# Kernel tuning notes

Hardware: AMD Instinct MI355X
Metric: run time of the kernel (lower is better)

The kernel has to match this reference:

```python
import jax, jax.numpy as jnp
import numpy as np

B, T, E = 2048, 200, 128
H1, H2 = 64, 32
NEG_INF = -(2.0 ** 32) + 1.0  # matches tf source's -2**32 + 1 padding value


def setup_inputs() -> dict:
    key = jax.random.key(0)
    ks = jax.random.split(key, 8)
    queries = jax.random.normal(ks[0], (B, E), dtype=jnp.float32)
    keys = jax.random.normal(ks[1], (B, T, E), dtype=jnp.float32)
    keys_id = jax.random.randint(ks[2], (B, T), 0, 2, dtype=jnp.int32)
    # Dense params: MLP input is concat([q,k,q-k,q*k]) -> 4*E = 512
    W1 = jax.random.normal(ks[3], (4 * E, H1), dtype=jnp.float32) * (1.0 / np.sqrt(4 * E))
    b1 = jnp.zeros((H1,), dtype=jnp.float32)
    W2 = jax.random.normal(ks[4], (H1, H2), dtype=jnp.float32) * (1.0 / np.sqrt(H1))
    b2 = jnp.zeros((H2,), dtype=jnp.float32)
    W3 = jax.random.normal(ks[5], (H2, 1), dtype=jnp.float32) * (1.0 / np.sqrt(H2))
    b3 = jnp.zeros((1,), dtype=jnp.float32)
    return {"queries": queries, "keys": keys, "keys_id": keys_id,
            "W1": W1, "b1": b1, "W2": W2, "b2": b2, "W3": W3, "b3": b3}


def reference(queries, keys, keys_id, W1, b1, W2, b2, W3, b3):
    # tile query over the time axis: [B,E] -> [B,T,E]
    q = jnp.broadcast_to(queries[:, None, :], keys.shape)
    # concat features: [B,T,4E]
    feat = jnp.concatenate([q, keys, q - keys, q * keys], axis=2)
    # small MLP scorer
    h = jax.nn.relu(jnp.einsum('btf,fh->bth', feat, W1) + b1)
    h = jax.nn.relu(jnp.einsum('bth,hk->btk', h, W2) + b2)
    weight = jnp.einsum('btk,ko->bto', h, W3) + b3  # [B,T,1]
    # masked softmax over time axis (padding id == 0)
    mask = (keys_id != 0)[:, :, None]  # [B,T,1]
    weight = jnp.where(mask, weight, jnp.float32(NEG_INF))
    weight = jax.nn.softmax(weight, axis=1)
    # weighted mean pooling (original uses reduce_mean, i.e. sum/T)
    return jnp.mean(weight * keys, axis=1)  # [B,E]
```

## Files before the change

### kernel.cpp

```cpp
#include <hip/hip_runtime.h>
#include <hip/hip_bf16.h>

#define NEG_INF_F (-4294967295.0f)

typedef __attribute__((ext_vector_type(8))) short bf16x8;
typedef __attribute__((ext_vector_type(4))) float f32x4;

__device__ __forceinline__ unsigned short f2bf(float x) {
    unsigned u = __float_as_uint(x);
    return (unsigned short)((u + 0x7fffu + ((u >> 16) & 1u)) >> 16);
}
__device__ __forceinline__ unsigned f2bf2(float a, float b) {
    __hip_bfloat162 h2 = __float22bfloat162_rn(make_float2(a, b));
    unsigned r; __builtin_memcpy(&r, &h2, 4); return r;
}
union FragU { unsigned u[4]; bf16x8 h; };

struct __align__(16) Smem {
    unsigned short Mt[64 * 128];
    unsigned short h1s[4][16 * 64];
    float q[128];
    float cpart[256];
    float Om[4][128];
    float mw[4], lw[4];
};

__global__ __launch_bounds__(256, 3)
void attn_fused(const float* __restrict__ Q,
                const float* __restrict__ Kg,
                const int*   __restrict__ kid,
                const float* __restrict__ W1,
                const float* __restrict__ b1,
                const float* __restrict__ W2,
                const float* __restrict__ b2,
                const float* __restrict__ W3,
                const float* __restrict__ b3,
                float* __restrict__ out)
{
    __shared__ Smem sm;
    const int b    = blockIdx.x;
    const int tid  = threadIdx.x;
    const int wave = tid >> 6;
    const int lane = tid & 63;
    const int l15  = lane & 15;
    const int quad = lane >> 4;

    if (tid < 128) sm.q[tid] = Q[b * 128 + tid];

    bf16x8 W2f[2][2];
    #pragma unroll
    for (int ks = 0; ks < 2; ++ks) {
        #pragma unroll
        for (int nt = 0; nt < 2; ++nt) {
            const int n = nt * 16 + l15;
            const int kb = ks * 32 + quad * 8;
            bf16x8 f;
            #pragma unroll
            for (int j = 0; j < 8; ++j) f[j] = (short)f2bf(W2[(kb + j) * 32 + n]);
            W2f[ks][nt] = f;
        }
    }
    const float w3a = W3[l15],  w3b = W3[16 + l15];
    const float b2a = b2[l15],  b2b = b2[16 + l15];
    const float b3v = b3[0];
    __syncthreads();

    {
        const int n  = tid & 63;
        const int ko = (tid >> 6) * 2;
        #pragma unroll
        for (int i = 0; i < 16; ++i) {
            const int k = i * 8 + ko;
            const float v0 = (W1[(128 + k) * 64 + n] - W1[(256 + k) * 64 + n])
                           + sm.q[k] * W1[(384 + k) * 64 + n];
            const float v1 = (W1[(129 + k) * 64 + n] - W1[(257 + k) * 64 + n])
                           + sm.q[k + 1] * W1[(385 + k) * 64 + n];
            const int g = (k >> 3) ^ (n & 15);
            *reinterpret_cast<unsigned*>(&sm.Mt[n * 128 + g * 8 + (k & 7)]) = f2bf2(v0, v1);
        }
    }
    {
        const int n = tid & 63, kc = tid >> 6;
        float acc = (kc == 0) ? b1[n] : 0.0f;
        #pragma unroll 4
        for (int i = 0; i < 32; ++i) {
            const int k = kc * 32 + i;
            acc += sm.q[k] * (W1[k * 64 + n] + W1[(256 + k) * 64 + n]);
        }
        sm.cpart[kc * 64 + n] = acc;
    }
    __syncthreads();

    float cn[4];
    #pragma unroll
    for (int nt = 0; nt < 4; ++nt) {
        const int n = nt * 16 + l15;
        cn[nt] = sm.cpart[n] + sm.cpart[64 + n] + sm.cpart[128 + n] + sm.cpart[192 + n];
    }

    const float* kbase = Kg + (size_t)b * 25600;
    unsigned short* h1w = &sm.h1s[wave][0];
    const f32x4 zero4 = {0.f, 0.f, 0.f, 0.f};

    float O[32];
    #pragma unroll
    for (int i = 0; i < 32; ++i) O[i] = 0.0f;
    float mrun = -__builtin_inff(), lrun = 0.0f;

    for (int tile = wave; tile < 13; tile += 4) {
        const int t0 = tile * 16;
        const int t  = t0 + l15;
        const int tr = min(t, 199);
        const float* kr = kbase + tr * 128;
        float4 ka[4], kb_[4];
        #pragma unroll
        for (int ks = 0; ks < 4; ++ks) {
            ka[ks]  = *reinterpret_cast<const float4*>(kr + ks * 32 + quad * 8);
            kb_[ks] = *reinterpret_cast<const float4*>(kr + ks * 32 + quad * 8 + 4);
        }
        const int kidv = kid[b * 200 + tr];

        f32x4 acc[4] = {zero4, zero4, zero4, zero4};
        #pragma unroll
        for (int ks = 0; ks < 4; ++ks) {
            FragU A;
            A.u[0] = f2bf2(ka[ks].x,  ka[ks].y);
            A.u[1] = f2bf2(ka[ks].z,  ka[ks].w);
            A.u[2] = f2bf2(kb_[ks].x, kb_[ks].y);
            A.u[3] = f2bf2(kb_[ks].z, kb_[ks].w);
            #pragma unroll
            for (int nt = 0; nt < 4; ++nt) {
                const int n = nt * 16 + l15;
                const int g = (ks * 4 + quad) ^ l15;
                const bf16x8 Bf = *reinterpret_cast<const bf16x8*>(&sm.Mt[n * 128 + g * 8]);
                acc[nt] = __builtin_amdgcn_mfma_f32_16x16x32_bf16(A.h, Bf, acc[nt], 0, 0, 0);
            }
        }
        #pragma unroll
        for (int nt = 0; nt < 4; ++nt) {
            const int n = nt * 16 + l15;
            #pragma unroll
            for (int r = 0; r < 4; ++r) {
                const int m = quad * 4 + r;
                const float h = fmaxf(acc[nt][r] + cn[nt], 0.0f);
                const int g = (n >> 3) ^ (m & 7);
                h1w[m * 64 + g * 8 + (n & 7)] = f2bf(h);
            }
        }
        f32x4 p0 = zero4, p1 = zero4;
        #pragma unroll
        for (int ks = 0; ks < 2; ++ks) {
            const int g = (ks * 4 + quad) ^ (l15 & 7);
            const bf16x8 A2l = *reinterpret_cast<const bf16x8*>(&h1w[l15 * 64 + g * 8]);
            p0 = __builtin_amdgcn_mfma_f32_16x16x32_bf16(A2l, W2f[ks][0], p0, 0, 0, 0);
            p1 = __builtin_amdgcn_mfma_f32_16x16x32_bf16(A2l, W2f[ks][1], p1, 0, 0, 0);
        }
        float sv[4];
        #pragma unroll
        for (int r = 0; r < 4; ++r)
            sv[r] = fmaxf(p0[r] + b2a, 0.f) * w3a + fmaxf(p1[r] + b2b, 0.f) * w3b;
        #pragma unroll
        for (int off = 1; off < 16; off <<= 1) {
            #pragma unroll
            for (int r = 0; r < 4; ++r) sv[r] += __shfl_xor(sv[r], off);
        }
        const int src = (l15 >> 2) * 16;
        const float s0 = __shfl(sv[0], src), s1 = __shfl(sv[1], src);
        const float s2 = __shfl(sv[2], src), s3 = __shfl(sv[3], src);
        const int rr = l15 & 3;
        const float sres = (rr == 0) ? s0 : (rr == 1) ? s1 : (rr == 2) ? s2 : s3;
        float x;
        if (t < 200) x = (kidv != 0) ? (sres + b3v) : NEG_INF_F;
        else         x = -__builtin_inff();
        float tmax = x;
        #pragma unroll
        for (int off = 1; off < 16; off <<= 1) tmax = fmaxf(tmax, __shfl_xor(tmax, off));
        const float mnew  = fmaxf(mrun, tmax);
        const float alpha = __expf(mrun - mnew);
        const float w     = __expf(x - mnew);
        float tsum = w;
        #pragma unroll
        for (int off = 1; off < 16; off <<= 1) tsum += __shfl_xor(tsum, off);
        lrun = lrun * alpha + tsum;
        mrun = mnew;
        #pragma unroll
        for (int ks = 0; ks < 4; ++ks) {
            O[ks*8+0] = fmaf(O[ks*8+0], alpha, w * ka[ks].x);
            O[ks*8+1] = fmaf(O[ks*8+1], alpha, w * ka[ks].y);
            O[ks*8+2] = fmaf(O[ks*8+2], alpha, w * ka[ks].z);
            O[ks*8+3] = fmaf(O[ks*8+3], alpha, w * ka[ks].w);
            O[ks*8+4] = fmaf(O[ks*8+4], alpha, w * kb_[ks].x);
            O[ks*8+5] = fmaf(O[ks*8+5], alpha, w * kb_[ks].y);
            O[ks*8+6] = fmaf(O[ks*8+6], alpha, w * kb_[ks].z);
            O[ks*8+7] = fmaf(O[ks*8+7], alpha, w * kb_[ks].w);
        }
    }

    #pragma unroll
    for (int off = 1; off < 16; off <<= 1) {
        #pragma unroll
        for (int i = 0; i < 32; ++i) O[i] += __shfl_xor(O[i], off);
    }
    if (l15 == 0) {
        #pragma unroll
        for (int ks = 0; ks < 4; ++ks) {
            *reinterpret_cast<float4*>(&sm.Om[wave][ks * 32 + quad * 8]) =
                make_float4(O[ks*8+0], O[ks*8+1], O[ks*8+2], O[ks*8+3]);
            *reinterpret_cast<float4*>(&sm.Om[wave][ks * 32 + quad * 8 + 4]) =
                make_float4(O[ks*8+4], O[ks*8+5], O[ks*8+6], O[ks*8+7]);
        }
    }
    if (lane == 0) { sm.mw[wave] = mrun; sm.lw[wave] = lrun; }
    __syncthreads();

    if (tid < 128) {
        const float M = fmaxf(fmaxf(sm.mw[0], sm.mw[1]), fmaxf(sm.mw[2], sm.mw[3]));
        float den = 0.f, val = 0.f;
        #pragma unroll
        for (int w = 0; w < 4; ++w) {
            const float a = __expf(sm.mw[w] - M);
            den += sm.lw[w] * a;
            val += sm.Om[w][tid] * a;
        }
        out[(size_t)b * 128 + tid] = val / (den * 200.0f);
    }
}

extern "C" void kernel_launch(void* const* d_in, const int* in_sizes, int n_in,
                              void* d_out, int out_size, void* d_ws, size_t ws_size,
                              hipStream_t stream) {
    (void)in_sizes; (void)n_in; (void)out_size; (void)d_ws; (void)ws_size;
    attn_fused<<<dim3(2048), dim3(256), 0, stream>>>(
        (const float*)d_in[0], (const float*)d_in[1], (const int*)d_in[2],
        (const float*)d_in[3], (const float*)d_in[4], (const float*)d_in[5],
        (const float*)d_in[6], (const float*)d_in[7], (const float*)d_in[8],
        (float*)d_out);
}
```

Measured before the change: 325.7 us.

## Split per-batch W1 folding into a precompute kernel and prefetch next key tile

The per-batch folded weight matrix (bf16, swizzled) and bias vector are now computed in a separate kernel and written to workspace. The main kernel copies them into LDS with vectorized loads instead of recomputing them from W1. The main loop also double-buffers the key tile in registers, loading the next tile before computing on the current one to hide global memory latency. The cost is a 16 KB per-batch round trip through global memory, a second kernel launch, and higher register pressure under a 3-waves occupancy bound.

```diff
diff --git a/kernel.cpp b/kernel.cpp
--- a/kernel.cpp
+++ b/kernel.cpp
@@ -16,26 +16,72 @@
 }
 union FragU { unsigned u[4]; bf16x8 h; };
 
+struct SmemA { float q[128]; float cpart[256]; };
+
+__global__ __launch_bounds__(256)
+void precompute_cm(const float* __restrict__ Q, const float* __restrict__ W1,
+                   const float* __restrict__ b1,
+                   float* __restrict__ c_all, unsigned short* __restrict__ M_all)
+{
+    __shared__ SmemA sm;
+    const int b = blockIdx.x;
+    const int tid = threadIdx.x;
+    if (tid < 128) sm.q[tid] = Q[b * 128 + tid];
+    __syncthreads();
+
+    {
+        const int n = tid & 63, kc = tid >> 6;
+        float acc = (kc == 0) ? b1[n] : 0.0f;
+        #pragma unroll 4
+        for (int i = 0; i < 32; ++i) {
+            const int k = kc * 32 + i;
+            acc += sm.q[k] * (W1[k * 64 + n] + W1[(256 + k) * 64 + n]);
+        }
+        sm.cpart[kc * 64 + n] = acc;
+    }
+
+    #pragma unroll
+    for (int i = 0; i < 4; ++i) {
+        const int pos = tid + i * 256;
+        const int n   = pos >> 4;
+        const int p   = pos & 15;
+        const int kb  = (p ^ (n & 15)) * 8;
+        unsigned u[4];
+        #pragma unroll
+        for (int j = 0; j < 4; ++j) {
+            const int k0 = kb + 2 * j, k1 = k0 + 1;
+            const float v0 = (W1[(128 + k0) * 64 + n] - W1[(256 + k0) * 64 + n])
+                           + sm.q[k0] * W1[(384 + k0) * 64 + n];
+            const float v1 = (W1[(128 + k1) * 64 + n] - W1[(256 + k1) * 64 + n])
+                           + sm.q[k1] * W1[(384 + k1) * 64 + n];
+            u[j] = f2bf2(v0, v1);
+        }
+        uint4 pk = make_uint4(u[0], u[1], u[2], u[3]);
+        *reinterpret_cast<uint4*>(&M_all[(size_t)b * 8192 + pos * 8]) = pk;
+    }
+    __syncthreads();
+    if (tid < 64)
+        c_all[b * 64 + tid] = sm.cpart[tid] + sm.cpart[64 + tid]
+                            + sm.cpart[128 + tid] + sm.cpart[192 + tid];
+}
+
 struct __align__(16) Smem {
     unsigned short Mt[64 * 128];
     unsigned short h1s[4][16 * 64];
-    float q[128];
-    float cpart[256];
     float Om[4][128];
     float mw[4], lw[4];
 };
 
 __global__ __launch_bounds__(256, 3)
-void attn_fused(const float* __restrict__ Q,
-                const float* __restrict__ Kg,
-                const int*   __restrict__ kid,
-                const float* __restrict__ W1,
-                const float* __restrict__ b1,
-                const float* __restrict__ W2,
-                const float* __restrict__ b2,
-                const float* __restrict__ W3,
-                const float* __restrict__ b3,
-                float* __restrict__ out)
+void attn_main(const float* __restrict__ Kg,
+               const int*   __restrict__ kid,
+               const float* __restrict__ W2,
+               const float* __restrict__ b2,
+               const float* __restrict__ W3,
+               const float* __restrict__ b3,
+               const float* __restrict__ c_all,
+               const unsigned short* __restrict__ M_all,
+               float* __restrict__ out)
 {
     __shared__ Smem sm;
     const int b    = blockIdx.x;
@@ -45,8 +91,14 @@
     const int l15  = lane & 15;
     const int quad = lane >> 4;
 
-    if (tid < 128) sm.q[tid] = Q[b * 128 + tid];
-
+    {
+        const uint4* msrc = reinterpret_cast<const uint4*>(M_all + (size_t)b * 8192);
+        #pragma unroll
+        for (int i = 0; i < 4; ++i) {
+            const int pos = tid + i * 256;
+            *reinterpret_cast<uint4*>(&sm.Mt[pos * 8]) = msrc[pos];
+        }
+    }
     bf16x8 W2f[2][2];
     #pragma unroll
     for (int ks = 0; ks < 2; ++ks) {
@@ -63,40 +115,10 @@
     const float w3a = W3[l15],  w3b = W3[16 + l15];
     const float b2a = b2[l15],  b2b = b2[16 + l15];
     const float b3v = b3[0];
-    __syncthreads();
-
-    {
-        const int n  = tid & 63;
-        const int ko = (tid >> 6) * 2;
-        #pragma unroll
-        for (int i = 0; i < 16; ++i) {
-            const int k = i * 8 + ko;
-            const float v0 = (W1[(128 + k) * 64 + n] - W1[(256 + k) * 64 + n])
-                           + sm.q[k] * W1[(384 + k) * 64 + n];
-            const float v1 = (W1[(129 + k) * 64 + n] - W1[(257 + k) * 64 + n])
-                           + sm.q[k + 1] * W1[(385 + k) * 64 + n];
-            const int g = (k >> 3) ^ (n & 15);
-            *reinterpret_cast<unsigned*>(&sm.Mt[n * 128 + g * 8 + (k & 7)]) = f2bf2(v0, v1);
-        }
-    }
-    {
-        const int n = tid & 63, kc = tid >> 6;
-        float acc = (kc == 0) ? b1[n] : 0.0f;
-        #pragma unroll 4
-        for (int i = 0; i < 32; ++i) {
-            const int k = kc * 32 + i;
-            acc += sm.q[k] * (W1[k * 64 + n] + W1[(256 + k) * 64 + n]);
-        }
-        sm.cpart[kc * 64 + n] = acc;
-    }
-    __syncthreads();
-
     float cn[4];
     #pragma unroll
-    for (int nt = 0; nt < 4; ++nt) {
-        const int n = nt * 16 + l15;
-        cn[nt] = sm.cpart[n] + sm.cpart[64 + n] + sm.cpart[128 + n] + sm.cpart[192 + n];
-    }
+    for (int nt = 0; nt < 4; ++nt) cn[nt] = c_all[b * 64 + nt * 16 + l15];
+    __syncthreads();
 
     const float* kbase = Kg + (size_t)b * 25600;
     unsigned short* h1w = &sm.h1s[wave][0];
@@ -107,27 +129,42 @@
     for (int i = 0; i < 32; ++i) O[i] = 0.0f;
     float mrun = -__builtin_inff(), lrun = 0.0f;
 
+    float4 kaA[4], kbA[4]; int kidA;
+    {
+        const int tr = min(wave * 16 + l15, 199);
+        const float* kr = kbase + tr * 128;
+        #pragma unroll
+        for (int ks = 0; ks < 4; ++ks) {
+            kaA[ks] = *reinterpret_cast<const float4*>(kr + ks * 32 + quad * 8);
+            kbA[ks] = *reinterpret_cast<const float4*>(kr + ks * 32 + quad * 8 + 4);
+        }
+        kidA = kid[b * 200 + tr];
+    }
+
     for (int tile = wave; tile < 13; tile += 4) {
+        float4 kaB[4], kbB[4]; int kidB = 0;
+        const int nx = tile + 4;
+        if (nx < 13) {
+            const int tr = min(nx * 16 + l15, 199);
+            const float* kr = kbase + tr * 128;
+            #pragma unroll
+            for (int ks = 0; ks < 4; ++ks) {
+                kaB[ks] = *reinterpret_cast<const float4*>(kr + ks * 32 + quad * 8);
+                kbB[ks] = *reinterpret_cast<const float4*>(kr + ks * 32 + quad * 8 + 4);
+            }
+            kidB = kid[b * 200 + tr];
+        }
+
         const int t0 = tile * 16;
         const int t  = t0 + l15;
-        const int tr = min(t, 199);
-        const float* kr = kbase + tr * 128;
-        float4 ka[4], kb_[4];
-        #pragma unroll
-        for (int ks = 0; ks < 4; ++ks) {
-            ka[ks]  = *reinterpret_cast<const float4*>(kr + ks * 32 + quad * 8);
-            kb_[ks] = *reinterpret_cast<const float4*>(kr + ks * 32 + quad * 8 + 4);
-        }
-        const int kidv = kid[b * 200 + tr];
-
         f32x4 acc[4] = {zero4, zero4, zero4, zero4};
         #pragma unroll
         for (int ks = 0; ks < 4; ++ks) {
             FragU A;
-            A.u[0] = f2bf2(ka[ks].x,  ka[ks].y);
-            A.u[1] = f2bf2(ka[ks].z,  ka[ks].w);
-            A.u[2] = f2bf2(kb_[ks].x, kb_[ks].y);
-            A.u[3] = f2bf2(kb_[ks].z, kb_[ks].w);
+            A.u[0] = f2bf2(kaA[ks].x, kaA[ks].y);
+            A.u[1] = f2bf2(kaA[ks].z, kaA[ks].w);
+            A.u[2] = f2bf2(kbA[ks].x, kbA[ks].y);
+            A.u[3] = f2bf2(kbA[ks].z, kbA[ks].w);
             #pragma unroll
             for (int nt = 0; nt < 4; ++nt) {
                 const int n = nt * 16 + l15;
@@ -170,7 +207,7 @@
         const int rr = l15 & 3;
         const float sres = (rr == 0) ? s0 : (rr == 1) ? s1 : (rr == 2) ? s2 : s3;
         float x;
-        if (t < 200) x = (kidv != 0) ? (sres + b3v) : NEG_INF_F;
+        if (t < 200) x = (kidA != 0) ? (sres + b3v) : NEG_INF_F;
         else         x = -__builtin_inff();
         float tmax = x;
         #pragma unroll
@@ -185,14 +222,19 @@
         mrun = mnew;
         #pragma unroll
         for (int ks = 0; ks < 4; ++ks) {
-            O[ks*8+0] = fmaf(O[ks*8+0], alpha, w * ka[ks].x);
-            O[ks*8+1] = fmaf(O[ks*8+1], alpha, w * ka[ks].y);
-            O[ks*8+2] = fmaf(O[ks*8+2], alpha, w * ka[ks].z);
-            O[ks*8+3] = fmaf(O[ks*8+3], alpha, w * ka[ks].w);
-            O[ks*8+4] = fmaf(O[ks*8+4], alpha, w * kb_[ks].x);
-            O[ks*8+5] = fmaf(O[ks*8+5], alpha, w * kb_[ks].y);
-            O[ks*8+6] = fmaf(O[ks*8+6], alpha, w * kb_[ks].z);
-            O[ks*8+7] = fmaf(O[ks*8+7], alpha, w * kb_[ks].w);
+            O[ks*8+0] = fmaf(O[ks*8+0], alpha, w * kaA[ks].x);
+            O[ks*8+1] = fmaf(O[ks*8+1], alpha, w * kaA[ks].y);
+            O[ks*8+2] = fmaf(O[ks*8+2], alpha, w * kaA[ks].z);
+            O[ks*8+3] = fmaf(O[ks*8+3], alpha, w * kaA[ks].w);
+            O[ks*8+4] = fmaf(O[ks*8+4], alpha, w * kbA[ks].x);
+            O[ks*8+5] = fmaf(O[ks*8+5], alpha, w * kbA[ks].y);
+            O[ks*8+6] = fmaf(O[ks*8+6], alpha, w * kbA[ks].z);
+            O[ks*8+7] = fmaf(O[ks*8+7], alpha, w * kbA[ks].w);
+        }
+        if (nx < 13) {
+            #pragma unroll
+            for (int ks = 0; ks < 4; ++ks) { kaA[ks] = kaB[ks]; kbA[ks] = kbB[ks]; }
+            kidA = kidB;
         }
     }
 
@@ -229,10 +271,16 @@
 extern "C" void kernel_launch(void* const* d_in, const int* in_sizes, int n_in,
                               void* d_out, int out_size, void* d_ws, size_t ws_size,
                               hipStream_t stream) {
-    (void)in_sizes; (void)n_in; (void)out_size; (void)d_ws; (void)ws_size;
-    attn_fused<<<dim3(2048), dim3(256), 0, stream>>>(
-        (const float*)d_in[0], (const float*)d_in[1], (const int*)d_in[2],
-        (const float*)d_in[3], (const float*)d_in[4], (const float*)d_in[5],
-        (const float*)d_in[6], (const float*)d_in[7], (const float*)d_in[8],
-        (float*)d_out);
-}
+    (void)in_sizes; (void)n_in; (void)out_size; (void)ws_size;
+    float*          c_all = (float*)d_ws;
+    unsigned short* M_all = (unsigned short*)((char*)d_ws + (1 << 19));
+
+    precompute_cm<<<dim3(2048), dim3(256), 0, stream>>>(
+        (const float*)d_in[0], (const float*)d_in[3], (const float*)d_in[4],
+        c_all, M_all);
+    attn_main<<<dim3(2048), dim3(256), 0, stream>>>(
+        (const float*)d_in[1], (const int*)d_in[2],
+        (const float*)d_in[5], (const float*)d_in[6],
+        (const float*)d_in[7], (const float*)d_in[8],
+        c_all, M_all, (float*)d_out);
+}
```

Measured after the change: 441.1 us. 35.4% more time.
